# Performance work log

Hardware: AMD Instinct MI355X
Metric: run time of the kernel (lower is better)

## Reference

```python
import jax, jax.numpy as jnp
import numpy as np

ALPHA = 0.2          # LeakyReLU negative slope
THRESHOLD = 0.5      # adjacency threshold
NEG_INF = -9e15      # same fill value as torch source


def setup_inputs() -> dict:
    key = jax.random.key(0)
    k_in, k_adj, k_W, k_a = jax.random.split(key, 4)
    B, N, C = 32, 1024, 64
    inp = jax.random.normal(k_in, (B, N, C), dtype=jnp.float32)
    adj = jax.random.uniform(k_adj, (N, N), dtype=jnp.float32)
    # xavier_uniform with gain=1.414 (as in torch init)
    gain = 1.414
    lim_W = gain * np.sqrt(6.0 / (C + C))
    W = jax.random.uniform(k_W, (C, C), dtype=jnp.float32, minval=-lim_W, maxval=lim_W)
    lim_a = gain * np.sqrt(6.0 / (2 * C + 1))
    a = jax.random.uniform(k_a, (2 * C, 1), dtype=jnp.float32, minval=-lim_a, maxval=lim_a)
    return {"input": inp, "adj": adj, "W": W, "a": a}


def reference(input, adj, W, a):
    # h: [B, N, C]
    h = jnp.matmul(input, W)
    C = W.shape[0]
    a_src = a[:C, 0]   # applied to h_i (row / query node)
    a_dst = a[C:, 0]   # applied to h_j (col / neighbor node)
    # Algebraic decomposition of a^T [h_i || h_j]: outer-sum of two [B,N] vectors.
    s_src = jnp.matmul(h, a_src)  # [B, N]
    s_dst = jnp.matmul(h, a_dst)  # [B, N]
    e = jax.nn.leaky_relu(s_src[:, :, None] + s_dst[:, None, :], negative_slope=ALPHA)  # [B,N,N]
    mask = adj > THRESHOLD  # [N, N], broadcast over batch
    attention = jax.nn.softmax(jnp.where(mask[None, :, :], e, NEG_INF), axis=2)
    h_prime = jnp.matmul(attention, h)  # [B, N, C]
    return jax.nn.elu(h_prime)
```

## Files before the change

### kernel.cpp

```cpp
#include <hip/hip_runtime.h>
#include <math.h>

#define ALPHA 0.2f
#define LOG2E 1.4426950408889634f

constexpr int B = 32, N = 1024, C = 64;
constexpr int TI = 32;

typedef __attribute__((ext_vector_type(8))) short short8;
typedef __attribute__((ext_vector_type(4))) float floatx4;

static __device__ __forceinline__ unsigned f32bf(float f) {
    unsigned u = __float_as_uint(f);
    return (u + 0x7FFFu + ((u >> 16) & 1u)) >> 16;
}

__global__ __launch_bounds__(256) void gat_mask(const float* __restrict__ adj,
                                                const float* __restrict__ Wm,
                                                const float* __restrict__ a,
                                                unsigned long long* __restrict__ mask64,
                                                float* __restrict__ wa)
{
    const int lane = threadIdx.x & 63;
    const int wave = threadIdx.x >> 6;
    const int id   = blockIdx.x * 4 + wave;
    const int i    = id >> 4;
    const int jc   = id & 15;
    const float av = adj[(size_t)i * N + jc * 64 + lane];
    const unsigned long long bal = __ballot(av > 0.5f);
    if (lane == 0) mask64[i * 16 + jc] = bal;

    if (blockIdx.x == 0 && wave == 0) {
        float accs = 0.f, accd = 0.f;
#pragma unroll
        for (int c4 = 0; c4 < 16; ++c4) {
            const float4 wv = *(const float4*)&Wm[lane * 64 + c4 * 4];
            const float4 as = *(const float4*)&a[c4 * 4];
            const float4 ad = *(const float4*)&a[64 + c4 * 4];
            accs = fmaf(wv.x, as.x, fmaf(wv.y, as.y, fmaf(wv.z, as.z, fmaf(wv.w, as.w, accs))));
            accd = fmaf(wv.x, ad.x, fmaf(wv.y, ad.y, fmaf(wv.z, ad.z, fmaf(wv.w, ad.w, accd))));
        }
        wa[lane] = accs;
        wa[64 + lane] = accd;
    }
}

__global__ __launch_bounds__(256) void gat_hs(const float* __restrict__ input,
                                              const float* __restrict__ Wm,
                                              const float* __restrict__ wa,
                                              unsigned short* __restrict__ hT2,
                                              float* __restrict__ ssrc,
                                              float* __restrict__ sdst)
{
    __shared__ __align__(16) float ins[64 * 68];
    __shared__ __align__(16) unsigned short hsT[64 * 72];
    __shared__ float red_s[256], red_d[256];
    __shared__ float wa_l[128];

    const int tid  = threadIdx.x;
    const int lane = tid & 63;
    const int wave = tid >> 6;
    const int row0 = blockIdx.x * 64;
    const int b    = row0 >> 10;
    const int jb   = row0 & 1023;

    float wreg[64];
#pragma unroll
    for (int k = 0; k < 64; ++k) wreg[k] = Wm[k * 64 + lane];

    const float4* gin = (const float4*)(input + (size_t)row0 * 64);
#pragma unroll
    for (int s = 0; s < 4; ++s) {
        const int id = tid + 256 * s;
        *(float4*)&ins[(id >> 4) * 68 + (id & 15) * 4] = gin[id];
    }
    if (tid < 128) wa_l[tid] = wa[tid];
    __syncthreads();

    for (int r = 0; r < 16; ++r) {
        const int row = wave * 16 + r;
        float acc = 0.f;
#pragma unroll
        for (int k4 = 0; k4 < 16; ++k4) {
            const float4 iv = *(const float4*)&ins[row * 68 + k4 * 4];
            acc = fmaf(iv.x, wreg[k4 * 4 + 0], acc);
            acc = fmaf(iv.y, wreg[k4 * 4 + 1], acc);
            acc = fmaf(iv.z, wreg[k4 * 4 + 2], acc);
            acc = fmaf(iv.w, wreg[k4 * 4 + 3], acc);
        }
        hsT[lane * 72 + row] = (unsigned short)f32bf(acc);
    }

    {
        const int r = tid & 63, kq = tid >> 6;
        float as = 0.f, ad = 0.f;
#pragma unroll
        for (int t = 0; t < 4; ++t) {
            const float4 iv = *(const float4*)&ins[r * 68 + kq * 16 + t * 4];
            const float4 ws = *(const float4*)&wa_l[kq * 16 + t * 4];
            const float4 wd = *(const float4*)&wa_l[64 + kq * 16 + t * 4];
            as = fmaf(iv.x, ws.x, fmaf(iv.y, ws.y, fmaf(iv.z, ws.z, fmaf(iv.w, ws.w, as))));
            ad = fmaf(iv.x, wd.x, fmaf(iv.y, wd.y, fmaf(iv.z, wd.z, fmaf(iv.w, wd.w, ad))));
        }
        red_s[tid] = as;
        red_d[tid] = ad;
    }
    __syncthreads();

    if (tid < 64) {
        ssrc[row0 + tid] = (red_s[tid] + red_s[tid + 64] + red_s[tid + 128] + red_s[tid + 192]) * LOG2E;
        sdst[row0 + tid] = (red_d[tid] + red_d[tid + 64] + red_d[tid + 128] + red_d[tid + 192]) * LOG2E;
    }

    {
        const int il2 = (tid & 7) * 2;
        const int fq  = (tid >> 3) & 3;
        const int cg  = (tid >> 5) & 3;
        const int t   = tid >> 7;
        const int c   = cg * 16 + il2;
        const int off = t * 32 + fq * 8;
        const short8 v0 = *(const short8*)&hsT[c * 72 + off];
        const short8 v1 = *(const short8*)&hsT[(c + 1) * 72 + off];
        unsigned short* g = hT2 + (((size_t)b * 16 + (jb >> 6)) << 12) + tid * 16;
        *(short8*)&g[0] = v0;
        *(short8*)&g[8] = v1;
    }
}

__global__ __launch_bounds__(256) void gat_attn(const unsigned short* __restrict__ hT2,
                                                const float* __restrict__ ssrc,
                                                const float* __restrict__ sdst,
                                                const unsigned* __restrict__ mask32,
                                                float* __restrict__ out)
{
    __shared__ __align__(16) float red[4][TI][68];
    __shared__ float pps[4][2][16];

    const int tid  = threadIdx.x;
    const int lane = tid & 63;
    const int w    = tid >> 6;
    const int b    = blockIdx.x >> 5;
    const int i0   = (blockIdx.x & 31) * TI;

    const int il = lane & 15;
    const int fq = lane >> 4;

    const float ssq0 = ssrc[b * N + i0 + il];
    const float ssq1 = ssrc[b * N + i0 + 16 + il];
    const float* sd = sdst + b * N;
    const unsigned* mb0 = mask32 + (size_t)(i0 + il) * 32;
    const unsigned* mb1 = mask32 + (size_t)(i0 + 16 + il) * 32;

    floatx4 acc[2][4];
#pragma unroll
    for (int ig = 0; ig < 2; ++ig)
#pragma unroll
        for (int cg = 0; cg < 4; ++cg) acc[ig][cg] = (floatx4){0.f, 0.f, 0.f, 0.f};
    float ps0 = 0.f, ps1 = 0.f;

    union Af { short8 v; unsigned u[4]; };

    for (int it = 0; it < 4; ++it) {
        const int jt = it * 4 + w;
        const float4 s0 = *(const float4*)&sd[jt * 64 + fq * 8];
        const float4 s1 = *(const float4*)&sd[jt * 64 + fq * 8 + 4];
        const float4 s2 = *(const float4*)&sd[jt * 64 + 32 + fq * 8];
        const float4 s3 = *(const float4*)&sd[jt * 64 + 32 + fq * 8 + 4];
        const uint2 m0 = *(const uint2*)&mb0[jt * 2];
        const uint2 m1 = *(const uint2*)&mb1[jt * 2];
        const unsigned short* hp = hT2 + (((size_t)b * 16 + jt) << 12) + lane * 8;
        short8 bf[4][2];
#pragma unroll
        for (int cg = 0; cg < 4; ++cg) {
            bf[cg][0] = *(const short8*)(hp + (0 * 4 + cg) * 512);
            bf[cg][1] = *(const short8*)(hp + (1 * 4 + cg) * 512);
        }

        float sv[16];
        *(float4*)&sv[0]  = s0;
        *(float4*)&sv[4]  = s1;
        *(float4*)&sv[8]  = s2;
        *(float4*)&sv[12] = s3;

        Af af[2][2];
#pragma unroll
        for (int ig = 0; ig < 2; ++ig) {
            const float ssq = ig ? ssq1 : ssq0;
            const uint2 mw = ig ? m1 : m0;
            float psl = 0.f;
#pragma unroll
            for (int t = 0; t < 2; ++t) {
                const unsigned mbits = (t ? mw.y : mw.x) >> (fq * 8);
                float p[8];
#pragma unroll
                for (int e = 0; e < 8; ++e) {
                    float x = ssq + sv[t * 8 + e];
                    x = fmaxf(x, ALPHA * x);
                    x = __builtin_amdgcn_exp2f(x);
                    p[e] = ((mbits >> e) & 1u) ? x : 0.f;
                }
                psl += ((p[0] + p[1]) + (p[2] + p[3])) + ((p[4] + p[5]) + (p[6] + p[7]));
#pragma unroll
                for (int q = 0; q < 4; ++q) {
                    unsigned r;
                    asm("v_cvt_pk_bf16_f32 %0, %1, %2" : "=v"(r) : "v"(p[q * 2]), "v"(p[q * 2 + 1]));
                    af[ig][t].u[q] = r;
                }
            }
            if (ig) ps1 += psl; else ps0 += psl;
        }

#pragma unroll
        for (int ig = 0; ig < 2; ++ig)
#pragma unroll
            for (int cg = 0; cg < 4; ++cg) {
                acc[ig][cg] = __builtin_amdgcn_mfma_f32_16x16x32_bf16(af[ig][0].v, bf[cg][0], acc[ig][cg], 0, 0, 0);
                acc[ig][cg] = __builtin_amdgcn_mfma_f32_16x16x32_bf16(af[ig][1].v, bf[cg][1], acc[ig][cg], 0, 0, 0);
            }
    }

    ps0 += __shfl_xor(ps0, 16); ps0 += __shfl_xor(ps0, 32);
    ps1 += __shfl_xor(ps1, 16); ps1 += __shfl_xor(ps1, 32);
    if (lane < 16) { pps[w][0][lane] = ps0; pps[w][1][lane] = ps1; }

#pragma unroll
    for (int ig = 0; ig < 2; ++ig)
#pragma unroll
        for (int cg = 0; cg < 4; ++cg)
#pragma unroll
            for (int r = 0; r < 4; ++r)
                red[w][ig * 16 + fq * 4 + r][cg * 16 + il] = acc[ig][cg][r];
    __syncthreads();

    const int row = tid >> 3;
    const int c0  = (tid & 7) * 8;
    float4 oa = {0.f, 0.f, 0.f, 0.f}, ob = {0.f, 0.f, 0.f, 0.f};
#pragma unroll
    for (int ww = 0; ww < 4; ++ww) {
        const float4 xa = *(const float4*)&red[ww][row][c0];
        const float4 xb = *(const float4*)&red[ww][row][c0 + 4];
        oa.x += xa.x; oa.y += xa.y; oa.z += xa.z; oa.w += xa.w;
        ob.x += xb.x; ob.y += xb.y; ob.z += xb.z; ob.w += xb.w;
    }
    const int ig = row >> 4, rl = row & 15;
    const float inv = 1.f / (pps[0][ig][rl] + pps[1][ig][rl] + pps[2][ig][rl] + pps[3][ig][rl]);
    float o[8] = {oa.x, oa.y, oa.z, oa.w, ob.x, ob.y, ob.z, ob.w};
#pragma unroll
    for (int e = 0; e < 8; ++e) {
        const float hp = o[e] * inv;
        o[e] = hp > 0.f ? hp : __expf(hp) - 1.f;
    }
    float* op = out + ((size_t)(b * N + i0 + row)) * 64 + c0;
    *(float4*)&op[0] = *(float4*)&o[0];
    *(float4*)&op[4] = *(float4*)&o[4];
}

extern "C" void kernel_launch(void* const* d_in, const int* in_sizes, int n_in,
                              void* d_out, int out_size, void* d_ws, size_t ws_size,
                              hipStream_t stream) {
    const float* input = (const float*)d_in[0];
    const float* adj   = (const float*)d_in[1];
    const float* Wm    = (const float*)d_in[2];
    const float* a     = (const float*)d_in[3];
    float* out = (float*)d_out;

    char* ws = (char*)d_ws;
    unsigned short* hT2 = (unsigned short*)ws;
    float* ssrc = (float*)(ws + 4194304);
    float* sdst = (float*)(ws + 4194304 + 131072);
    unsigned long long* mask64 = (unsigned long long*)(ws + 4194304 + 2 * 131072);
    float* wa = (float*)(ws + 4194304 + 3 * 131072);

    gat_mask<<<N * N / 64 / 4, 256, 0, stream>>>(adj, Wm, a, mask64, wa);
    gat_hs<<<B * N / 64, 256, 0, stream>>>(input, Wm, wa, hT2, ssrc, sdst);
    gat_attn<<<B * (N / TI), 256, 0, stream>>>(hT2, ssrc, sdst, (const unsigned*)mask64, out);
}
```

Baseline: 90.38 us.

## Factor exp of leaky-relu scores into products and fuse prep kernels

Precomputes exp2 of the source and destination scores, plus of the scores scaled by the slope, in the prep kernel. Since exp2 is monotonic, exp2(leaky(s+d)) equals max(Es*Ed, Es2*Ed2), so the attention kernel does multiplies and a max instead of a transcendental per pair. The mask, W·a and h kernels are merged into one launch, and the attention tile grows to 64 rows with a swizzled block order for better reuse of h. Risks include overflow when scores are large (no max subtraction), higher register pressure from 16 accumulators, and fewer blocks.

```diff
diff --git a/kernel.cpp b/kernel.cpp
--- a/kernel.cpp
+++ b/kernel.cpp
@@ -4,8 +4,8 @@
 #define ALPHA 0.2f
 #define LOG2E 1.4426950408889634f
 
-constexpr int B = 32, N = 1024, C = 64;
-constexpr int TI = 32;
+constexpr int B = 32, N = 1024;
+constexpr int TI = 64;
 
 typedef __attribute__((ext_vector_type(8))) short short8;
 typedef __attribute__((ext_vector_type(4))) float floatx4;
@@ -15,22 +15,51 @@
     return (u + 0x7FFFu + ((u >> 16) & 1u)) >> 16;
 }
 
-__global__ __launch_bounds__(256) void gat_mask(const float* __restrict__ adj,
-                                                const float* __restrict__ Wm,
-                                                const float* __restrict__ a,
-                                                unsigned long long* __restrict__ mask64,
-                                                float* __restrict__ wa)
+__global__ __launch_bounds__(256) void gat_pre(const float* __restrict__ input,
+                                               const float* __restrict__ adj,
+                                               const float* __restrict__ Wm,
+                                               const float* __restrict__ a,
+                                               unsigned short* __restrict__ hT2,
+                                               unsigned long long* __restrict__ mask64,
+                                               float* __restrict__ es,
+                                               float* __restrict__ es2,
+                                               float* __restrict__ ed,
+                                               float* __restrict__ ed2)
 {
-    const int lane = threadIdx.x & 63;
-    const int wave = threadIdx.x >> 6;
-    const int id   = blockIdx.x * 4 + wave;
-    const int i    = id >> 4;
-    const int jc   = id & 15;
-    const float av = adj[(size_t)i * N + jc * 64 + lane];
-    const unsigned long long bal = __ballot(av > 0.5f);
-    if (lane == 0) mask64[i * 16 + jc] = bal;
-
-    if (blockIdx.x == 0 && wave == 0) {
+    const int tid  = threadIdx.x;
+    const int lane = tid & 63;
+    const int wave = tid >> 6;
+
+    if (blockIdx.x >= 512) {
+        const int id = (blockIdx.x - 512) * 4 + wave;
+        const int i  = id >> 4;
+        const int jc = id & 15;
+        const float av = adj[(size_t)i * N + jc * 64 + lane];
+        const unsigned long long bal = __ballot(av > 0.5f);
+        if (lane == 0) mask64[i * 16 + jc] = bal;
+        return;
+    }
+
+    __shared__ __align__(16) float ins[64 * 68];
+    __shared__ __align__(16) unsigned short hsT[64 * 72];
+    __shared__ float red_s[256], red_d[256];
+    __shared__ float wa_l[128];
+
+    const int row0 = blockIdx.x * 64;
+    const int b    = row0 >> 10;
+    const int jb   = row0 & 1023;
+
+    float wreg[64];
+#pragma unroll
+    for (int k = 0; k < 64; ++k) wreg[k] = Wm[k * 64 + lane];
+
+    const float4* gin = (const float4*)(input + (size_t)row0 * 64);
+#pragma unroll
+    for (int s = 0; s < 4; ++s) {
+        const int id = tid + 256 * s;
+        *(float4*)&ins[(id >> 4) * 68 + (id & 15) * 4] = gin[id];
+    }
+    if (wave == 0) {
         float accs = 0.f, accd = 0.f;
 #pragma unroll
         for (int c4 = 0; c4 < 16; ++c4) {
@@ -40,41 +69,9 @@
             accs = fmaf(wv.x, as.x, fmaf(wv.y, as.y, fmaf(wv.z, as.z, fmaf(wv.w, as.w, accs))));
             accd = fmaf(wv.x, ad.x, fmaf(wv.y, ad.y, fmaf(wv.z, ad.z, fmaf(wv.w, ad.w, accd))));
         }
-        wa[lane] = accs;
-        wa[64 + lane] = accd;
-    }
-}
-
-__global__ __launch_bounds__(256) void gat_hs(const float* __restrict__ input,
-                                              const float* __restrict__ Wm,
-                                              const float* __restrict__ wa,
-                                              unsigned short* __restrict__ hT2,
-                                              float* __restrict__ ssrc,
-                                              float* __restrict__ sdst)
-{
-    __shared__ __align__(16) float ins[64 * 68];
-    __shared__ __align__(16) unsigned short hsT[64 * 72];
-    __shared__ float red_s[256], red_d[256];
-    __shared__ float wa_l[128];
-
-    const int tid  = threadIdx.x;
-    const int lane = tid & 63;
-    const int wave = tid >> 6;
-    const int row0 = blockIdx.x * 64;
-    const int b    = row0 >> 10;
-    const int jb   = row0 & 1023;
-
-    float wreg[64];
-#pragma unroll
-    for (int k = 0; k < 64; ++k) wreg[k] = Wm[k * 64 + lane];
-
-    const float4* gin = (const float4*)(input + (size_t)row0 * 64);
-#pragma unroll
-    for (int s = 0; s < 4; ++s) {
-        const int id = tid + 256 * s;
-        *(float4*)&ins[(id >> 4) * 68 + (id & 15) * 4] = gin[id];
-    }
-    if (tid < 128) wa_l[tid] = wa[tid];
+        wa_l[lane] = accs;
+        wa_l[64 + lane] = accd;
+    }
     __syncthreads();
 
     for (int r = 0; r < 16; ++r) {
@@ -108,8 +105,12 @@
     __syncthreads();
 
     if (tid < 64) {
-        ssrc[row0 + tid] = (red_s[tid] + red_s[tid + 64] + red_s[tid + 128] + red_s[tid + 192]) * LOG2E;
-        sdst[row0 + tid] = (red_d[tid] + red_d[tid + 64] + red_d[tid + 128] + red_d[tid + 192]) * LOG2E;
+        const float ss = (red_s[tid] + red_s[tid + 64] + red_s[tid + 128] + red_s[tid + 192]) * LOG2E;
+        const float dd = (red_d[tid] + red_d[tid + 64] + red_d[tid + 128] + red_d[tid + 192]) * LOG2E;
+        es [row0 + tid] = __builtin_amdgcn_exp2f(ss);
+        es2[row0 + tid] = __builtin_amdgcn_exp2f(0.2f * ss);
+        ed [row0 + tid] = __builtin_amdgcn_exp2f(dd);
+        ed2[row0 + tid] = __builtin_amdgcn_exp2f(0.2f * dd);
     }
 
     {
@@ -128,103 +129,106 @@
 }
 
 __global__ __launch_bounds__(256) void gat_attn(const unsigned short* __restrict__ hT2,
-                                                const float* __restrict__ ssrc,
-                                                const float* __restrict__ sdst,
+                                                const float* __restrict__ es,
+                                                const float* __restrict__ es2,
+                                                const float* __restrict__ ed,
+                                                const float* __restrict__ ed2,
                                                 const unsigned* __restrict__ mask32,
                                                 float* __restrict__ out)
 {
-    __shared__ __align__(16) float red[4][TI][68];
-    __shared__ float pps[4][2][16];
+    __shared__ __align__(16) float red[4][64][68];
+    __shared__ float pps[4][4][16];
 
     const int tid  = threadIdx.x;
     const int lane = tid & 63;
     const int w    = tid >> 6;
-    const int b    = blockIdx.x >> 5;
-    const int i0   = (blockIdx.x & 31) * TI;
-
-    const int il = lane & 15;
-    const int fq = lane >> 4;
-
-    const float ssq0 = ssrc[b * N + i0 + il];
-    const float ssq1 = ssrc[b * N + i0 + 16 + il];
-    const float* sd = sdst + b * N;
-    const unsigned* mb0 = mask32 + (size_t)(i0 + il) * 32;
-    const unsigned* mb1 = mask32 + (size_t)(i0 + 16 + il) * 32;
-
-    floatx4 acc[2][4];
-#pragma unroll
-    for (int ig = 0; ig < 2; ++ig)
+    const int bid  = (blockIdx.x & 7) * 64 + (blockIdx.x >> 3);
+    const int b    = bid >> 4;
+    const int i0   = (bid & 15) * TI;
+
+    const int il  = lane & 15;
+    const int fq  = lane >> 4;
+    const int fsh = fq * 8;
+
+    float E[4], E2[4];
+#pragma unroll
+    for (int ig = 0; ig < 4; ++ig) {
+        E[ig]  = es [b * N + i0 + ig * 16 + il];
+        E2[ig] = es2[b * N + i0 + ig * 16 + il];
+    }
+    const float* edb  = ed  + b * N;
+    const float* ed2b = ed2 + b * N;
+
+    floatx4 acc[4][4];
+#pragma unroll
+    for (int ig = 0; ig < 4; ++ig)
 #pragma unroll
         for (int cg = 0; cg < 4; ++cg) acc[ig][cg] = (floatx4){0.f, 0.f, 0.f, 0.f};
-    float ps0 = 0.f, ps1 = 0.f;
+    float ps[4] = {0.f, 0.f, 0.f, 0.f};
 
     union Af { short8 v; unsigned u[4]; };
 
     for (int it = 0; it < 4; ++it) {
         const int jt = it * 4 + w;
-        const float4 s0 = *(const float4*)&sd[jt * 64 + fq * 8];
-        const float4 s1 = *(const float4*)&sd[jt * 64 + fq * 8 + 4];
-        const float4 s2 = *(const float4*)&sd[jt * 64 + 32 + fq * 8];
-        const float4 s3 = *(const float4*)&sd[jt * 64 + 32 + fq * 8 + 4];
-        const uint2 m0 = *(const uint2*)&mb0[jt * 2];
-        const uint2 m1 = *(const uint2*)&mb1[jt * 2];
         const unsigned short* hp = hT2 + (((size_t)b * 16 + jt) << 12) + lane * 8;
-        short8 bf[4][2];
-#pragma unroll
-        for (int cg = 0; cg < 4; ++cg) {
-            bf[cg][0] = *(const short8*)(hp + (0 * 4 + cg) * 512);
-            bf[cg][1] = *(const short8*)(hp + (1 * 4 + cg) * 512);
-        }
-
-        float sv[16];
-        *(float4*)&sv[0]  = s0;
-        *(float4*)&sv[4]  = s1;
-        *(float4*)&sv[8]  = s2;
-        *(float4*)&sv[12] = s3;
-
-        Af af[2][2];
-#pragma unroll
-        for (int ig = 0; ig < 2; ++ig) {
-            const float ssq = ig ? ssq1 : ssq0;
-            const uint2 mw = ig ? m1 : m0;
-            float psl = 0.f;
-#pragma unroll
-            for (int t = 0; t < 2; ++t) {
-                const unsigned mbits = (t ? mw.y : mw.x) >> (fq * 8);
+        uint2 m[4];
+#pragma unroll
+        for (int ig = 0; ig < 4; ++ig)
+            m[ig] = *(const uint2*)&mask32[(size_t)(i0 + ig * 16 + il) * 32 + jt * 2];
+
+#pragma unroll
+        for (int t = 0; t < 2; ++t) {
+            const int j0 = jt * 64 + t * 32 + fsh;
+            const float4 d0 = *(const float4*)&edb[j0];
+            const float4 d1 = *(const float4*)&edb[j0 + 4];
+            const float4 g0 = *(const float4*)&ed2b[j0];
+            const float4 g1 = *(const float4*)&ed2b[j0 + 4];
+            short8 bf[4];
+#pragma unroll
+            for (int cg = 0; cg < 4; ++cg)
+                bf[cg] = *(const short8*)(hp + (t * 4 + cg) * 512);
+
+            float dv[8], gv[8];
+            *(float4*)&dv[0] = d0; *(float4*)&dv[4] = d1;
+            *(float4*)&gv[0] = g0; *(float4*)&gv[4] = g1;
+
+            Af af[4];
+#pragma unroll
+            for (int ig = 0; ig < 4; ++ig) {
+                const unsigned mbits = (t ? m[ig].y : m[ig].x) >> fsh;
                 float p[8];
 #pragma unroll
                 for (int e = 0; e < 8; ++e) {
-                    float x = ssq + sv[t * 8 + e];
-                    x = fmaxf(x, ALPHA * x);
-                    x = __builtin_amdgcn_exp2f(x);
+                    const float x = fmaxf(E[ig] * dv[e], E2[ig] * gv[e]);
                     p[e] = ((mbits >> e) & 1u) ? x : 0.f;
                 }
-                psl += ((p[0] + p[1]) + (p[2] + p[3])) + ((p[4] + p[5]) + (p[6] + p[7]));
+                ps[ig] += ((p[0] + p[1]) + (p[2] + p[3])) + ((p[4] + p[5]) + (p[6] + p[7]));
 #pragma unroll
                 for (int q = 0; q < 4; ++q) {
                     unsigned r;
                     asm("v_cvt_pk_bf16_f32 %0, %1, %2" : "=v"(r) : "v"(p[q * 2]), "v"(p[q * 2 + 1]));
-                    af[ig][t].u[q] = r;
+                    af[ig].u[q] = r;
                 }
             }
-            if (ig) ps1 += psl; else ps0 += psl;
-        }
-
-#pragma unroll
-        for (int ig = 0; ig < 2; ++ig)
-#pragma unroll
-            for (int cg = 0; cg < 4; ++cg) {
-                acc[ig][cg] = __builtin_amdgcn_mfma_f32_16x16x32_bf16(af[ig][0].v, bf[cg][0], acc[ig][cg], 0, 0, 0);
-                acc[ig][cg] = __builtin_amdgcn_mfma_f32_16x16x32_bf16(af[ig][1].v, bf[cg][1], acc[ig][cg], 0, 0, 0);
-            }
-    }
-
-    ps0 += __shfl_xor(ps0, 16); ps0 += __shfl_xor(ps0, 32);
-    ps1 += __shfl_xor(ps1, 16); ps1 += __shfl_xor(ps1, 32);
-    if (lane < 16) { pps[w][0][lane] = ps0; pps[w][1][lane] = ps1; }
-
-#pragma unroll
-    for (int ig = 0; ig < 2; ++ig)
+#pragma unroll
+            for (int ig = 0; ig < 4; ++ig)
+#pragma unroll
+                for (int cg = 0; cg < 4; ++cg)
+                    acc[ig][cg] = __builtin_amdgcn_mfma_f32_16x16x32_bf16(af[ig].v, bf[cg], acc[ig][cg], 0, 0, 0);
+        }
+    }
+
+#pragma unroll
+    for (int ig = 0; ig < 4; ++ig) {
+        ps[ig] += __shfl_xor(ps[ig], 16);
+        ps[ig] += __shfl_xor(ps[ig], 32);
+    }
+    if (lane < 16)
+#pragma unroll
+        for (int ig = 0; ig < 4; ++ig) pps[w][ig][lane] = ps[ig];
+
+#pragma unroll
+    for (int ig = 0; ig < 4; ++ig)
 #pragma unroll
         for (int cg = 0; cg < 4; ++cg)
 #pragma unroll
@@ -232,27 +236,27 @@
                 red[w][ig * 16 + fq * 4 + r][cg * 16 + il] = acc[ig][cg][r];
     __syncthreads();
 
-    const int row = tid >> 3;
-    const int c0  = (tid & 7) * 8;
-    float4 oa = {0.f, 0.f, 0.f, 0.f}, ob = {0.f, 0.f, 0.f, 0.f};
-#pragma unroll
-    for (int ww = 0; ww < 4; ++ww) {
-        const float4 xa = *(const float4*)&red[ww][row][c0];
-        const float4 xb = *(const float4*)&red[ww][row][c0 + 4];
-        oa.x += xa.x; oa.y += xa.y; oa.z += xa.z; oa.w += xa.w;
-        ob.x += xb.x; ob.y += xb.y; ob.z += xb.z; ob.w += xb.w;
-    }
-    const int ig = row >> 4, rl = row & 15;
+    const int row = tid >> 2;
+    const int c0  = (tid & 3) * 16;
+    const int ig  = row >> 4, rl = row & 15;
     const float inv = 1.f / (pps[0][ig][rl] + pps[1][ig][rl] + pps[2][ig][rl] + pps[3][ig][rl]);
-    float o[8] = {oa.x, oa.y, oa.z, oa.w, ob.x, ob.y, ob.z, ob.w};
-#pragma unroll
-    for (int e = 0; e < 8; ++e) {
-        const float hp = o[e] * inv;
-        o[e] = hp > 0.f ? hp : __expf(hp) - 1.f;
-    }
     float* op = out + ((size_t)(b * N + i0 + row)) * 64 + c0;
-    *(float4*)&op[0] = *(float4*)&o[0];
-    *(float4*)&op[4] = *(float4*)&o[4];
+#pragma unroll
+    for (int q = 0; q < 4; ++q) {
+        const float4 v0 = *(const float4*)&red[0][row][c0 + q * 4];
+        const float4 v1 = *(const float4*)&red[1][row][c0 + q * 4];
+        const float4 v2 = *(const float4*)&red[2][row][c0 + q * 4];
+        const float4 v3 = *(const float4*)&red[3][row][c0 + q * 4];
+        float o[4];
+        o[0] = ((v0.x + v1.x) + (v2.x + v3.x)) * inv;
+        o[1] = ((v0.y + v1.y) + (v2.y + v3.y)) * inv;
+        o[2] = ((v0.z + v1.z) + (v2.z + v3.z)) * inv;
+        o[3] = ((v0.w + v1.w) + (v2.w + v3.w)) * inv;
+#pragma unroll
+        for (int e = 0; e < 4; ++e)
+            o[e] = o[e] > 0.f ? o[e] : __expf(o[e]) - 1.f;
+        *(float4*)&op[q * 4] = *(const float4*)&o[0];
+    }
 }
 
 extern "C" void kernel_launch(void* const* d_in, const int* in_sizes, int n_in,
@@ -266,12 +270,14 @@
 
     char* ws = (char*)d_ws;
     unsigned short* hT2 = (unsigned short*)ws;
-    float* ssrc = (float*)(ws + 4194304);
-    float* sdst = (float*)(ws + 4194304 + 131072);
-    unsigned long long* mask64 = (unsigned long long*)(ws + 4194304 + 2 * 131072);
-    float* wa = (float*)(ws + 4194304 + 3 * 131072);
-
-    gat_mask<<<N * N / 64 / 4, 256, 0, stream>>>(adj, Wm, a, mask64, wa);
-    gat_hs<<<B * N / 64, 256, 0, stream>>>(input, Wm, wa, hT2, ssrc, sdst);
-    gat_attn<<<B * (N / TI), 256, 0, stream>>>(hT2, ssrc, sdst, (const unsigned*)mask64, out);
-}
+    float* es  = (float*)(ws + 4194304);
+    float* es2 = (float*)(ws + 4194304 + 131072);
+    float* ed  = (float*)(ws + 4194304 + 2 * 131072);
+    float* ed2 = (float*)(ws + 4194304 + 3 * 131072);
+    unsigned long long* mask64 = (unsigned long long*)(ws + 4194304 + 4 * 131072);
+
+    gat_pre<<<512 + N * N / 64 / 4, 256, 0, stream>>>(input, adj, Wm, a, hT2, mask64,
+                                                      es, es2, ed, ed2);
+    gat_attn<<<B * (N / TI), 256, 0, stream>>>(hT2, es, es2, ed, ed2,
+                                               (const unsigned*)mask64, out);
+}
```

Result: slower. 95.32 us (+5.5%).

## Factor per-pair exponential into precomputed per-node exponentials with max

Applied to the files above, without the earlier changes.

Because exp is monotonic, exp(leaky(s+d)) equals max(e^s·e^d, e^{0.2s}·e^{0.2d}). The producer kernel now writes four per-node exponential arrays, and the attention kernel builds each score from two multiplies and a max instead of an add, a leaky max and an exp2 per element. The attention kernel also swizzles the block index across XCD groups and splits the j-tile loop into two halves, which shrinks the live B-fragment and score registers. The cost is twice the per-neighbour loads and a risk of overflow or precision change, since the product of exponentials is formed without a max-subtraction.

```diff
diff --git a/kernel.cpp b/kernel.cpp
--- a/kernel.cpp
+++ b/kernel.cpp
@@ -4,7 +4,7 @@
 #define ALPHA 0.2f
 #define LOG2E 1.4426950408889634f
 
-constexpr int B = 32, N = 1024, C = 64;
+constexpr int B = 32, N = 1024;
 constexpr int TI = 32;
 
 typedef __attribute__((ext_vector_type(8))) short short8;
@@ -49,8 +49,10 @@
                                               const float* __restrict__ Wm,
                                               const float* __restrict__ wa,
                                               unsigned short* __restrict__ hT2,
-                                              float* __restrict__ ssrc,
-                                              float* __restrict__ sdst)
+                                              float* __restrict__ es,
+                                              float* __restrict__ es2,
+                                              float* __restrict__ ed,
+                                              float* __restrict__ ed2)
 {
     __shared__ __align__(16) float ins[64 * 68];
     __shared__ __align__(16) unsigned short hsT[64 * 72];
@@ -108,8 +110,12 @@
     __syncthreads();
 
     if (tid < 64) {
-        ssrc[row0 + tid] = (red_s[tid] + red_s[tid + 64] + red_s[tid + 128] + red_s[tid + 192]) * LOG2E;
-        sdst[row0 + tid] = (red_d[tid] + red_d[tid + 64] + red_d[tid + 128] + red_d[tid + 192]) * LOG2E;
+        const float ss = (red_s[tid] + red_s[tid + 64] + red_s[tid + 128] + red_s[tid + 192]) * LOG2E;
+        const float dd = (red_d[tid] + red_d[tid + 64] + red_d[tid + 128] + red_d[tid + 192]) * LOG2E;
+        es [row0 + tid] = __builtin_amdgcn_exp2f(ss);
+        es2[row0 + tid] = __builtin_amdgcn_exp2f(0.2f * ss);
+        ed [row0 + tid] = __builtin_amdgcn_exp2f(dd);
+        ed2[row0 + tid] = __builtin_amdgcn_exp2f(0.2f * dd);
     }
 
     {
@@ -128,8 +134,10 @@
 }
 
 __global__ __launch_bounds__(256) void gat_attn(const unsigned short* __restrict__ hT2,
-                                                const float* __restrict__ ssrc,
-                                                const float* __restrict__ sdst,
+                                                const float* __restrict__ es,
+                                                const float* __restrict__ es2,
+                                                const float* __restrict__ ed,
+                                                const float* __restrict__ ed2,
                                                 const unsigned* __restrict__ mask32,
                                                 float* __restrict__ out)
 {
@@ -139,15 +147,20 @@
     const int tid  = threadIdx.x;
     const int lane = tid & 63;
     const int w    = tid >> 6;
-    const int b    = blockIdx.x >> 5;
-    const int i0   = (blockIdx.x & 31) * TI;
-
-    const int il = lane & 15;
-    const int fq = lane >> 4;
-
-    const float ssq0 = ssrc[b * N + i0 + il];
-    const float ssq1 = ssrc[b * N + i0 + 16 + il];
-    const float* sd = sdst + b * N;
+    const int bid  = (blockIdx.x & 7) * 128 + (blockIdx.x >> 3);
+    const int b    = bid >> 5;
+    const int i0   = (bid & 31) * TI;
+
+    const int il  = lane & 15;
+    const int fq  = lane >> 4;
+    const int fsh = fq * 8;
+
+    const float E0  = es [b * N + i0 + il];
+    const float E1  = es [b * N + i0 + 16 + il];
+    const float F0  = es2[b * N + i0 + il];
+    const float F1  = es2[b * N + i0 + 16 + il];
+    const float* edb  = ed  + b * N;
+    const float* ed2b = ed2 + b * N;
     const unsigned* mb0 = mask32 + (size_t)(i0 + il) * 32;
     const unsigned* mb1 = mask32 + (size_t)(i0 + 16 + il) * 32;
 
@@ -162,61 +175,54 @@
 
     for (int it = 0; it < 4; ++it) {
         const int jt = it * 4 + w;
-        const float4 s0 = *(const float4*)&sd[jt * 64 + fq * 8];
-        const float4 s1 = *(const float4*)&sd[jt * 64 + fq * 8 + 4];
-        const float4 s2 = *(const float4*)&sd[jt * 64 + 32 + fq * 8];
-        const float4 s3 = *(const float4*)&sd[jt * 64 + 32 + fq * 8 + 4];
+        const unsigned short* hp = hT2 + (((size_t)b * 16 + jt) << 12) + lane * 8;
         const uint2 m0 = *(const uint2*)&mb0[jt * 2];
         const uint2 m1 = *(const uint2*)&mb1[jt * 2];
-        const unsigned short* hp = hT2 + (((size_t)b * 16 + jt) << 12) + lane * 8;
-        short8 bf[4][2];
-#pragma unroll
-        for (int cg = 0; cg < 4; ++cg) {
-            bf[cg][0] = *(const short8*)(hp + (0 * 4 + cg) * 512);
-            bf[cg][1] = *(const short8*)(hp + (1 * 4 + cg) * 512);
-        }
-
-        float sv[16];
-        *(float4*)&sv[0]  = s0;
-        *(float4*)&sv[4]  = s1;
-        *(float4*)&sv[8]  = s2;
-        *(float4*)&sv[12] = s3;
-
-        Af af[2][2];
-#pragma unroll
-        for (int ig = 0; ig < 2; ++ig) {
-            const float ssq = ig ? ssq1 : ssq0;
-            const uint2 mw = ig ? m1 : m0;
-            float psl = 0.f;
-#pragma unroll
-            for (int t = 0; t < 2; ++t) {
-                const unsigned mbits = (t ? mw.y : mw.x) >> (fq * 8);
+
+#pragma unroll
+        for (int t = 0; t < 2; ++t) {
+            const int j0 = jt * 64 + t * 32 + fsh;
+            const float4 d0 = *(const float4*)&edb[j0];
+            const float4 d1 = *(const float4*)&edb[j0 + 4];
+            const float4 g0 = *(const float4*)&ed2b[j0];
+            const float4 g1 = *(const float4*)&ed2b[j0 + 4];
+            short8 bf[4];
+#pragma unroll
+            for (int cg = 0; cg < 4; ++cg)
+                bf[cg] = *(const short8*)(hp + (t * 4 + cg) * 512);
+
+            float dv[8], gv[8];
+            *(float4*)&dv[0] = d0; *(float4*)&dv[4] = d1;
+            *(float4*)&gv[0] = g0; *(float4*)&gv[4] = g1;
+
+            Af af[2];
+#pragma unroll
+            for (int ig = 0; ig < 2; ++ig) {
+                const float E  = ig ? E1 : E0;
+                const float F  = ig ? F1 : F0;
+                const uint2 mw = ig ? m1 : m0;
+                const unsigned mbits = (t ? mw.y : mw.x) >> fsh;
                 float p[8];
 #pragma unroll
                 for (int e = 0; e < 8; ++e) {
-                    float x = ssq + sv[t * 8 + e];
-                    x = fmaxf(x, ALPHA * x);
-                    x = __builtin_amdgcn_exp2f(x);
+                    const float x = fmaxf(E * dv[e], F * gv[e]);
                     p[e] = ((mbits >> e) & 1u) ? x : 0.f;
                 }
-                psl += ((p[0] + p[1]) + (p[2] + p[3])) + ((p[4] + p[5]) + (p[6] + p[7]));
+                const float psl = ((p[0] + p[1]) + (p[2] + p[3])) + ((p[4] + p[5]) + (p[6] + p[7]));
+                if (ig) ps1 += psl; else ps0 += psl;
 #pragma unroll
                 for (int q = 0; q < 4; ++q) {
                     unsigned r;
                     asm("v_cvt_pk_bf16_f32 %0, %1, %2" : "=v"(r) : "v"(p[q * 2]), "v"(p[q * 2 + 1]));
-                    af[ig][t].u[q] = r;
+                    af[ig].u[q] = r;
                 }
             }
-            if (ig) ps1 += psl; else ps0 += psl;
-        }
-
-#pragma unroll
-        for (int ig = 0; ig < 2; ++ig)
-#pragma unroll
-            for (int cg = 0; cg < 4; ++cg) {
-                acc[ig][cg] = __builtin_amdgcn_mfma_f32_16x16x32_bf16(af[ig][0].v, bf[cg][0], acc[ig][cg], 0, 0, 0);
-                acc[ig][cg] = __builtin_amdgcn_mfma_f32_16x16x32_bf16(af[ig][1].v, bf[cg][1], acc[ig][cg], 0, 0, 0);
-            }
+#pragma unroll
+            for (int ig = 0; ig < 2; ++ig)
+#pragma unroll
+                for (int cg = 0; cg < 4; ++cg)
+                    acc[ig][cg] = __builtin_amdgcn_mfma_f32_16x16x32_bf16(af[ig].v, bf[cg], acc[ig][cg], 0, 0, 0);
+        }
     }
 
     ps0 += __shfl_xor(ps0, 16); ps0 += __shfl_xor(ps0, 32);
@@ -266,12 +272,15 @@
 
     char* ws = (char*)d_ws;
     unsigned short* hT2 = (unsigned short*)ws;
-    float* ssrc = (float*)(ws + 4194304);
-    float* sdst = (float*)(ws + 4194304 + 131072);
-    unsigned long long* mask64 = (unsigned long long*)(ws + 4194304 + 2 * 131072);
-    float* wa = (float*)(ws + 4194304 + 3 * 131072);
+    float* es  = (float*)(ws + 4194304);
+    float* es2 = (float*)(ws + 4194304 + 131072);
+    float* ed  = (float*)(ws + 4194304 + 2 * 131072);
+    float* ed2 = (float*)(ws + 4194304 + 3 * 131072);
+    unsigned long long* mask64 = (unsigned long long*)(ws + 4194304 + 4 * 131072);
+    float* wa = (float*)(ws + 4194304 + 5 * 131072);
 
     gat_mask<<<N * N / 64 / 4, 256, 0, stream>>>(adj, Wm, a, mask64, wa);
-    gat_hs<<<B * N / 64, 256, 0, stream>>>(input, Wm, wa, hT2, ssrc, sdst);
-    gat_attn<<<B * (N / TI), 256, 0, stream>>>(hT2, ssrc, sdst, (const unsigned*)mask64, out);
-}
+    gat_hs<<<B * N / 64, 256, 0, stream>>>(input, Wm, wa, hT2, es, es2, ed, ed2);
+    gat_attn<<<B * (N / TI), 256, 0, stream>>>(hT2, es, es2, ed, ed2,
+                                               (const unsigned*)mask64, out);
+}
```

New measurement: 94.08 us. +4.1%, slower.

## Fuse adjacency mask and W·a precompute into the projection kernel

Applied to the files above, without the earlier changes.

Removes the separate gat_mask launch. Each gat_hs block now builds 32 mask words from adj by ballot and computes W·a locally into shared memory instead of reading it from a workspace buffer. This saves one kernel launch and the global round-trip for wa. In exchange every block repeats the small W·a product, and the adj loads add register pressure to the projection kernel.

```diff
diff --git a/kernel.cpp b/kernel.cpp
--- a/kernel.cpp
+++ b/kernel.cpp
@@ -4,7 +4,7 @@
 #define ALPHA 0.2f
 #define LOG2E 1.4426950408889634f
 
-constexpr int B = 32, N = 1024, C = 64;
+constexpr int B = 32, N = 1024;
 constexpr int TI = 32;
 
 typedef __attribute__((ext_vector_type(8))) short short8;
@@ -15,22 +15,46 @@
     return (u + 0x7FFFu + ((u >> 16) & 1u)) >> 16;
 }
 
-__global__ __launch_bounds__(256) void gat_mask(const float* __restrict__ adj,
-                                                const float* __restrict__ Wm,
-                                                const float* __restrict__ a,
-                                                unsigned long long* __restrict__ mask64,
-                                                float* __restrict__ wa)
+__global__ __launch_bounds__(256) void gat_hs(const float* __restrict__ input,
+                                              const float* __restrict__ adj,
+                                              const float* __restrict__ Wm,
+                                              const float* __restrict__ a,
+                                              unsigned short* __restrict__ hT2,
+                                              float* __restrict__ ssrc,
+                                              float* __restrict__ sdst,
+                                              unsigned long long* __restrict__ mask64)
 {
-    const int lane = threadIdx.x & 63;
-    const int wave = threadIdx.x >> 6;
-    const int id   = blockIdx.x * 4 + wave;
-    const int i    = id >> 4;
-    const int jc   = id & 15;
-    const float av = adj[(size_t)i * N + jc * 64 + lane];
-    const unsigned long long bal = __ballot(av > 0.5f);
-    if (lane == 0) mask64[i * 16 + jc] = bal;
-
-    if (blockIdx.x == 0 && wave == 0) {
+    __shared__ __align__(16) float ins[64 * 68];
+    __shared__ __align__(16) unsigned short hsT[64 * 72];
+    __shared__ float red_s[256], red_d[256];
+    __shared__ float wa_l[128];
+
+    const int tid  = threadIdx.x;
+    const int lane = tid & 63;
+    const int wave = tid >> 6;
+    const int row0 = blockIdx.x * 64;
+    const int b    = row0 >> 10;
+    const int jb   = row0 & 1023;
+
+    const int unit0 = blockIdx.x * 32 + wave * 8;
+    float av[8];
+#pragma unroll
+    for (int k = 0; k < 8; ++k) {
+        const int u = unit0 + k;
+        av[k] = adj[((size_t)(u >> 4) << 10) + (u & 15) * 64 + lane];
+    }
+
+    float wreg[64];
+#pragma unroll
+    for (int k = 0; k < 64; ++k) wreg[k] = Wm[k * 64 + lane];
+
+    const float4* gin = (const float4*)(input + (size_t)row0 * 64);
+#pragma unroll
+    for (int s = 0; s < 4; ++s) {
+        const int id = tid + 256 * s;
+        *(float4*)&ins[(id >> 4) * 68 + (id & 15) * 4] = gin[id];
+    }
+    if (wave == 0) {
         float accs = 0.f, accd = 0.f;
 #pragma unroll
         for (int c4 = 0; c4 < 16; ++c4) {
@@ -40,41 +64,9 @@
             accs = fmaf(wv.x, as.x, fmaf(wv.y, as.y, fmaf(wv.z, as.z, fmaf(wv.w, as.w, accs))));
             accd = fmaf(wv.x, ad.x, fmaf(wv.y, ad.y, fmaf(wv.z, ad.z, fmaf(wv.w, ad.w, accd))));
         }
-        wa[lane] = accs;
-        wa[64 + lane] = accd;
-    }
-}
-
-__global__ __launch_bounds__(256) void gat_hs(const float* __restrict__ input,
-                                              const float* __restrict__ Wm,
-                                              const float* __restrict__ wa,
-                                              unsigned short* __restrict__ hT2,
-                                              float* __restrict__ ssrc,
-                                              float* __restrict__ sdst)
-{
-    __shared__ __align__(16) float ins[64 * 68];
-    __shared__ __align__(16) unsigned short hsT[64 * 72];
-    __shared__ float red_s[256], red_d[256];
-    __shared__ float wa_l[128];
-
-    const int tid  = threadIdx.x;
-    const int lane = tid & 63;
-    const int wave = tid >> 6;
-    const int row0 = blockIdx.x * 64;
-    const int b    = row0 >> 10;
-    const int jb   = row0 & 1023;
-
-    float wreg[64];
-#pragma unroll
-    for (int k = 0; k < 64; ++k) wreg[k] = Wm[k * 64 + lane];
-
-    const float4* gin = (const float4*)(input + (size_t)row0 * 64);
-#pragma unroll
-    for (int s = 0; s < 4; ++s) {
-        const int id = tid + 256 * s;
-        *(float4*)&ins[(id >> 4) * 68 + (id & 15) * 4] = gin[id];
-    }
-    if (tid < 128) wa_l[tid] = wa[tid];
+        wa_l[lane] = accs;
+        wa_l[64 + lane] = accd;
+    }
     __syncthreads();
 
     for (int r = 0; r < 16; ++r) {
@@ -125,6 +117,13 @@
         *(short8*)&g[0] = v0;
         *(short8*)&g[8] = v1;
     }
+
+#pragma unroll
+    for (int k = 0; k < 8; ++k) {
+        const int u = unit0 + k;
+        const unsigned long long bal = __ballot(av[k] > 0.5f);
+        if (lane == 0) mask64[(u >> 4) * 16 + (u & 15)] = bal;
+    }
 }
 
 __global__ __launch_bounds__(256) void gat_attn(const unsigned short* __restrict__ hT2,
@@ -269,9 +268,7 @@
     float* ssrc = (float*)(ws + 4194304);
     float* sdst = (float*)(ws + 4194304 + 131072);
     unsigned long long* mask64 = (unsigned long long*)(ws + 4194304 + 2 * 131072);
-    float* wa = (float*)(ws + 4194304 + 3 * 131072);
-
-    gat_mask<<<N * N / 64 / 4, 256, 0, stream>>>(adj, Wm, a, mask64, wa);
-    gat_hs<<<B * N / 64, 256, 0, stream>>>(input, Wm, wa, hT2, ssrc, sdst);
+
+    gat_hs<<<B * N / 64, 256, 0, stream>>>(input, adj, Wm, a, hT2, ssrc, sdst, mask64);
     gat_attn<<<B * (N / TI), 256, 0, stream>>>(hT2, ssrc, sdst, (const unsigned*)mask64, out);
 }
```

Result: no change. 89.79 us (-0.6%).
